# Kernel tuning notes

Hardware: AMD Instinct MI355X
Metric: run time of the kernel (lower is better)

The kernel has to match this reference:

```python
import jax, jax.numpy as jnp
import numpy as np

T, B, H, I = 128, 128, 256, 256


def setup_inputs() -> dict:
    key = jax.random.key(0)
    ks = jax.random.split(key, 8)
    s = 1.0 / np.sqrt(H)
    embs = jax.random.normal(ks[0], (T, B, I), jnp.float32)
    # lens in [1, T] (a length of 0 is meaningless for this module)
    lens = jnp.maximum(jax.random.randint(ks[1], (B,), 0, T + 1), 1)
    Wih = jax.random.uniform(ks[2], (4 * H, I), jnp.float32, -s, s)
    Whh = jax.random.uniform(ks[3], (4 * H, H), jnp.float32, -s, s)
    bih = jax.random.uniform(ks[4], (4 * H,), jnp.float32, -s, s)
    bhh = jax.random.uniform(ks[5], (4 * H,), jnp.float32, -s, s)
    Wa = jax.random.uniform(ks[6], (H, 2 * H), jnp.float32, -s, s)
    ba = jnp.zeros((H,), jnp.float32)
    return {"embs": embs, "lens": lens, "Wih": Wih, "Whh": Whh,
            "bih": bih, "bhh": bhh, "Wa": Wa, "ba": ba}


def _forward(embs, Wih, Whh, bih, bhh, Wa, ba):
    Tn, Bn, _ = embs.shape
    Hn = Whh.shape[1]
    h0 = jnp.zeros((Bn, Hn), embs.dtype)
    c0 = jnp.zeros((Bn, Hn), embs.dtype)
    hids0 = jnp.zeros((Tn, Bn, Hn), embs.dtype)  # growing history of outputs
    pos = jnp.arange(Tn)

    def step(carry, emb):
        h, c, hids, t = carry
        # attention of current hidden over all previous outputs (dot-product scores)
        scores = jnp.einsum('bh,tbh->tb', h, hids)          # [T,B]
        valid = pos[:, None] < jnp.maximum(t, 1)             # at least one valid slot avoids NaN
        scores = jnp.where(valid, scores, -1e30)
        w = jax.nn.softmax(scores, axis=0)
        ctx = jnp.einsum('tb,tbh->bh', w, hids)              # [B,H]
        h_att = jnp.tanh(jnp.concatenate([h, ctx], axis=-1) @ Wa.T + ba)
        h_in = jnp.where(t > 0, h_att, h)                    # no attention before first output
        # one LSTM cell step (PyTorch gate order: i, f, g, o)
        gates = emb @ Wih.T + bih + h_in @ Whh.T + bhh       # [B,4H]
        i, f, g, o = jnp.split(gates, 4, axis=-1)
        c_new = jax.nn.sigmoid(f) * c + jax.nn.sigmoid(i) * jnp.tanh(g)
        h_new = jax.nn.sigmoid(o) * jnp.tanh(c_new)
        hids = jax.lax.dynamic_update_slice(hids, h_new[None], (t, 0, 0))
        return (h_new, c_new, hids, t + 1), (h_new, c_new)

    _, (hs, cs) = jax.lax.scan(step, (h0, c0, hids0, jnp.int32(0)), embs)
    return hs, cs  # each [T,B,H]


def reference(embs, lens, Wih, Whh, bih, bhh, Wa, ba):
    hs, cs = _forward(embs, Wih, Whh, bih, bhh, Wa, ba)
    bidx = jnp.arange(hs.shape[1])
    h_fin = hs[lens - 1, bidx][None]  # [1,B,H], state at t == len-1
    c_fin = cs[lens - 1, bidx][None]
    return hs, h_fin, c_fin
```

## Files before the change

kernel.cpp:

```cpp
#include <hip/hip_runtime.h>
#include <math.h>

#define T 128
#define B 128
#define H 256
#define I 256
#define G4 1024
#define NB 2

typedef unsigned short u16;
typedef unsigned int u32;

__device__ __forceinline__ float2 bf2_to_f2(u32 u) {
    union { u32 i; float f; } a, b;
    a.i = u << 16;
    b.i = u & 0xffff0000u;
    return make_float2(a.f, b.f);
}
__device__ __forceinline__ float bf1_to_f(u16 u) {
    union { u32 i; float f; } a; a.i = ((u32)u) << 16; return a.f;
}
__device__ __forceinline__ u16 bf16_rne(float f) {
    union { float f; u32 u; } x; x.f = f;
    u32 r = x.u + 0x7fffu + ((x.u >> 16) & 1u);
    return (u16)(r >> 16);
}
__device__ __forceinline__ float sigmoid_fast(float x) {
    return 1.0f / (1.0f + __expf(-x));
}
__device__ __forceinline__ float tanh_fast(float x) {
    x = fminf(fmaxf(x, -15.f), 15.f);
    const float e = __expf(2.0f * x);
    return (e - 1.0f) / (e + 1.0f);
}

__global__ void pack_whB(const float* __restrict__ Whh, u16* __restrict__ WhB) {
    const int k = blockIdx.x;
    const int o = threadIdx.x;
    WhB[(size_t)k * G4 + o] = bf16_rne(Whh[(size_t)o * H + k]);
}
__global__ void pack_waB(const float* __restrict__ Wa, u16* __restrict__ WaB) {
    const int k = blockIdx.x;
    const int j = threadIdx.x;
    WaB[(size_t)k * H + j] = bf16_rne(Wa[(size_t)j * (2 * H) + k]);
}

__global__ __launch_bounds__(256) void gemm_g(const float* __restrict__ A,
                                              const float* __restrict__ W,
                                              const float* __restrict__ bih,
                                              const float* __restrict__ bhh,
                                              float* __restrict__ G) {
    __shared__ __align__(16) float As[64][68];
    __shared__ __align__(16) float Ws[64][68];
    const int m0 = blockIdx.x * 64;
    const int n0 = blockIdx.y * 64;
    const int tid = threadIdx.x;
    const int ty = tid >> 4, tx = tid & 15;
    const int rr = tid >> 4;
    const int kr = tid & 15;

    float acc[4][4] = {};
    for (int k0 = 0; k0 < I; k0 += 64) {
#pragma unroll
        for (int i = 0; i < 4; ++i) {
            const int r = rr + 16 * i;
            const float4 av = *(const float4*)&A[(size_t)(m0 + r) * I + k0 + kr * 4];
            const float4 wv = *(const float4*)&W[(size_t)(n0 + r) * I + k0 + kr * 4];
            As[kr * 4 + 0][r] = av.x; As[kr * 4 + 1][r] = av.y;
            As[kr * 4 + 2][r] = av.z; As[kr * 4 + 3][r] = av.w;
            Ws[kr * 4 + 0][r] = wv.x; Ws[kr * 4 + 1][r] = wv.y;
            Ws[kr * 4 + 2][r] = wv.z; Ws[kr * 4 + 3][r] = wv.w;
        }
        __syncthreads();
#pragma unroll 8
        for (int kk = 0; kk < 64; ++kk) {
            const float4 a4 = *(const float4*)&As[kk][ty * 4];
            const float4 w4 = *(const float4*)&Ws[kk][tx * 4];
            const float a[4] = {a4.x, a4.y, a4.z, a4.w};
            const float w[4] = {w4.x, w4.y, w4.z, w4.w};
#pragma unroll
            for (int i = 0; i < 4; ++i)
#pragma unroll
                for (int jj = 0; jj < 4; ++jj)
                    acc[i][jj] = fmaf(a[i], w[jj], acc[i][jj]);
        }
        __syncthreads();
    }
    const int n = n0 + tx * 4;
    const float4 bi = *(const float4*)&bih[n];
    const float4 bh = *(const float4*)&bhh[n];
    const float4 bb = make_float4(bi.x + bh.x, bi.y + bh.y, bi.z + bh.z, bi.w + bh.w);
#pragma unroll
    for (int i = 0; i < 4; ++i) {
        const int m = m0 + ty * 4 + i;
        float4 o = make_float4(acc[i][0] + bb.x, acc[i][1] + bb.y,
                               acc[i][2] + bb.z, acc[i][3] + bb.w);
        *(float4*)&G[(size_t)m * G4 + n] = o;
    }
}

__global__ __launch_bounds__(1024, 4) void alstm3(
    const int* __restrict__ lens,
    const float* __restrict__ G,
    const u16* __restrict__ WhB,
    const u16* __restrict__ WaB,
    const float* __restrict__ ba,
    float* __restrict__ out)
{
    __shared__ __align__(16) u16   hid_s[NB][T][H];
    __shared__ __align__(16) float red_s[4096];
    __shared__ __align__(16) float gate_s[NB][G4];
    __shared__ __align__(16) float h_s[NB][H];
    __shared__ __align__(16) float hin_s[NB][H];
    __shared__ __align__(16) float ctx_s[NB][H];
    __shared__ __align__(16) float sc_s[NB][T];

    const int b0 = blockIdx.x * NB;
    const int tid = threadIdx.x;
    const int lane = tid & 63;
    const int wave = tid >> 6;
    const int sb = wave >> 3;
    const int stp0 = wave & 7;
    const int cb = tid >> 9;
    const int ck = (tid >> 8) & 1;
    const int cj = tid & 255;
    const int ako = tid >> 7;
    const int aj = (tid & 127) * 2;
    const int hko = tid >> 9;
    const int ho = (tid & 511) * 2;
    const int eb = tid >> 8;
    const int ej = tid & 255;

    const int len0 = lens[b0], len1 = lens[b0 + 1];
    float c_reg = 0.f;
    if (tid < NB * H) h_s[eb][ej] = 0.f;
    float* hfin = out + (size_t)T * B * H;
    float* cfin = hfin + (size_t)B * H;
    __syncthreads();

    for (int t = 0; t < T; ++t) {
        const float gA = G[((size_t)t * B + b0) * G4 + tid];
        const float gB = G[((size_t)t * B + b0 + 1) * G4 + tid];

        if (t > 0) {
            const float4 h4 = *(const float4*)&h_s[sb][lane * 4];
            for (int tp = stp0; tp < t; tp += 8) {
                const uint2 hv = *(const uint2*)&hid_s[sb][tp][lane * 4];
                const float2 ha = bf2_to_f2(hv.x);
                const float2 hb = bf2_to_f2(hv.y);
                float d = ha.x * h4.x + ha.y * h4.y + hb.x * h4.z + hb.y * h4.w;
#pragma unroll
                for (int off = 32; off; off >>= 1) d += __shfl_xor(d, off);
                if (lane == 0) sc_s[sb][tp] = d;
            }
            __syncthreads();
            if (stp0 == 0) {
                const float v0 = (lane < t) ? sc_s[sb][lane] : -3.0e38f;
                const float v1 = (lane + 64 < t) ? sc_s[sb][lane + 64] : -3.0e38f;
                float m = fmaxf(v0, v1);
#pragma unroll
                for (int off = 32; off; off >>= 1) m = fmaxf(m, __shfl_xor(m, off));
                const float e0 = (lane < t) ? __expf(v0 - m) : 0.f;
                const float e1 = (lane + 64 < t) ? __expf(v1 - m) : 0.f;
                float s = e0 + e1;
#pragma unroll
                for (int off = 32; off; off >>= 1) s += __shfl_xor(s, off);
                const float inv = 1.f / s;
                if (lane < t) sc_s[sb][lane] = e0 * inv;
                if (lane + 64 < t) sc_s[sb][lane + 64] = e1 * inv;
            }
            __syncthreads();
            {
                float cacc = 0.f;
#pragma unroll 4
                for (int tp = ck; tp < t; tp += 2)
                    cacc = fmaf(sc_s[cb][tp], bf1_to_f(hid_s[cb][tp][cj]), cacc);
                red_s[cb * 512 + ck * 256 + cj] = cacc;
                gate_s[0][tid] = gA;
                gate_s[1][tid] = gB;
            }
            __syncthreads();
            if (tid < 512)
                ctx_s[eb][ej] = red_s[eb * 512 + ej] + red_s[eb * 512 + 256 + ej];
            __syncthreads();
            {
                const float* base0 = (ako < 4) ? &h_s[0][ako * 64] : &ctx_s[0][ako * 64 - 256];
                const float* base1 = (ako < 4) ? &h_s[1][ako * 64] : &ctx_s[1][ako * 64 - 256];
                const u16* wp = &WaB[(size_t)(ako * 64) * H + aj];
                float a00 = 0.f, a01 = 0.f, a10 = 0.f, a11 = 0.f;
#pragma unroll 8
                for (int kk = 0; kk < 64; ++kk) {
                    const u32 w = *(const u32*)(wp + (size_t)kk * H);
                    const float2 wv = bf2_to_f2(w);
                    const float v0 = base0[kk];
                    const float v1 = base1[kk];
                    a00 = fmaf(wv.x, v0, a00); a01 = fmaf(wv.y, v0, a01);
                    a10 = fmaf(wv.x, v1, a10); a11 = fmaf(wv.y, v1, a11);
                }
                *(float2*)&red_s[ako * 512 + aj] = make_float2(a00, a01);
                *(float2*)&red_s[ako * 512 + 256 + aj] = make_float2(a10, a11);
            }
            __syncthreads();
            if (tid < 512) {
                float a = ba[ej];
#pragma unroll
                for (int r = 0; r < 8; ++r) a += red_s[r * 512 + eb * 256 + ej];
                hin_s[eb][ej] = tanh_fast(a);
            }
            __syncthreads();
        } else {
            gate_s[0][tid] = gA;
            gate_s[1][tid] = gB;
            if (tid < 512) hin_s[eb][ej] = 0.f;
            __syncthreads();
        }
        {
            const u16* wp = &WhB[(size_t)(hko * 128) * G4 + ho];
            float a00 = 0.f, a01 = 0.f, a10 = 0.f, a11 = 0.f;
#pragma unroll 8
            for (int kk = 0; kk < 128; ++kk) {
                const int k = hko * 128 + kk;
                const u32 w = *(const u32*)(wp + (size_t)kk * G4);
                const float2 wv = bf2_to_f2(w);
                const float h0 = hin_s[0][k];
                const float h1 = hin_s[1][k];
                a00 = fmaf(wv.x, h0, a00); a01 = fmaf(wv.y, h0, a01);
                a10 = fmaf(wv.x, h1, a10); a11 = fmaf(wv.y, h1, a11);
            }
            *(float2*)&red_s[hko * 2048 + ho] = make_float2(a00, a01);
            *(float2*)&red_s[hko * 2048 + 1024 + ho] = make_float2(a10, a11);
        }
        __syncthreads();
        if (tid < 512) {
            const int bg = b0 + eb;
            const float gi = gate_s[eb][ej] + red_s[eb * 1024 + ej] + red_s[2048 + eb * 1024 + ej];
            const float gf = gate_s[eb][H + ej] + red_s[eb * 1024 + H + ej] + red_s[2048 + eb * 1024 + H + ej];
            const float gg = gate_s[eb][2 * H + ej] + red_s[eb * 1024 + 2 * H + ej] + red_s[2048 + eb * 1024 + 2 * H + ej];
            const float go = gate_s[eb][3 * H + ej] + red_s[eb * 1024 + 3 * H + ej] + red_s[2048 + eb * 1024 + 3 * H + ej];
            const float ig = sigmoid_fast(gi);
            const float fg = sigmoid_fast(gf);
            const float gv = tanh_fast(gg);
            const float og = sigmoid_fast(go);
            c_reg = fmaf(fg, c_reg, ig * gv);
            const float h_new = og * tanh_fast(c_reg);
            h_s[eb][ej] = h_new;
            hid_s[eb][t][ej] = bf16_rne(h_new);
            out[((size_t)t * B + bg) * H + ej] = h_new;
            const int lb = eb ? len1 : len0;
            if (t == lb - 1) {
                hfin[(size_t)bg * H + ej] = h_new;
                cfin[(size_t)bg * H + ej] = c_reg;
            }
        }
        __syncthreads();
    }
}

extern "C" void kernel_launch(void* const* d_in, const int* in_sizes, int n_in,
                              void* d_out, int out_size, void* d_ws, size_t ws_size,
                              hipStream_t stream) {
    const float* embs = (const float*)d_in[0];
    const int*   lens = (const int*)d_in[1];
    const float* Wih  = (const float*)d_in[2];
    const float* Whh  = (const float*)d_in[3];
    const float* bih  = (const float*)d_in[4];
    const float* bhh  = (const float*)d_in[5];
    const float* Wa   = (const float*)d_in[6];
    const float* ba   = (const float*)d_in[7];
    float* out = (float*)d_out;

    float* G  = (float*)d_ws;
    u16* WhB  = (u16*)(G + (size_t)T * B * G4);
    u16* WaB  = WhB + (size_t)H * G4;

    pack_whB<<<H, G4, 0, stream>>>(Whh, WhB);
    pack_waB<<<2 * H, H, 0, stream>>>(Wa, WaB);
    dim3 ggrid(T * B / 64, G4 / 64);
    gemm_g<<<ggrid, 256, 0, stream>>>(embs, Wih, bih, bhh, G);
    alstm3<<<B / NB, 1024, 0, stream>>>(lens, G, WhB, WaB, ba, out);
}
```

Baseline: 2.043 ms.

## Switch recurrent weights and history to fp16 with packed dot2 instructions

Replaces the bf16 storage of recurrent weights, attention weights and hidden history with fp16 pairs packed along the reduction dimension. The matvecs now use the v_dot2 fp32-accumulate instruction, with activations interleaved for the two batch rows so that one weight load serves both. Each thread covers a full output column, which removes the split-K partial sums and shrinks the reduction buffer. This cuts ALU work and bf16 unpacking per step, in exchange for fp16 range and precision limits on weights and hidden states.

```diff
diff --git a/kernel.cpp b/kernel.cpp
--- a/kernel.cpp
+++ b/kernel.cpp
@@ -10,21 +10,24 @@
 
 typedef unsigned short u16;
 typedef unsigned int u32;
-
-__device__ __forceinline__ float2 bf2_to_f2(u32 u) {
-    union { u32 i; float f; } a, b;
-    a.i = u << 16;
-    b.i = u & 0xffff0000u;
-    return make_float2(a.f, b.f);
-}
-__device__ __forceinline__ float bf1_to_f(u16 u) {
-    union { u32 i; float f; } a; a.i = ((u32)u) << 16; return a.f;
-}
-__device__ __forceinline__ u16 bf16_rne(float f) {
-    union { float f; u32 u; } x; x.f = f;
-    u32 r = x.u + 0x7fffu + ((x.u >> 16) & 1u);
-    return (u16)(r >> 16);
-}
+typedef _Float16 half_t;
+typedef _Float16 half2_t __attribute__((ext_vector_type(2)));
+
+#if defined(__has_builtin)
+#if __has_builtin(__builtin_amdgcn_fdot2)
+#define HAS_FDOT2 1
+#endif
+#endif
+
+__device__ __forceinline__ float fdot2(half2_t a, half2_t b, float c) {
+#ifdef HAS_FDOT2
+    return __builtin_amdgcn_fdot2(a, b, c, false);
+#else
+    return fmaf((float)a.x, (float)b.x, fmaf((float)a.y, (float)b.y, c));
+#endif
+}
+__device__ __forceinline__ half2_t h2cast(u32 u) { return __builtin_bit_cast(half2_t, u); }
+
 __device__ __forceinline__ float sigmoid_fast(float x) {
     return 1.0f / (1.0f + __expf(-x));
 }
@@ -34,15 +37,21 @@
     return (e - 1.0f) / (e + 1.0f);
 }
 
-__global__ void pack_whB(const float* __restrict__ Whh, u16* __restrict__ WhB) {
-    const int k = blockIdx.x;
-    const int o = threadIdx.x;
-    WhB[(size_t)k * G4 + o] = bf16_rne(Whh[(size_t)o * H + k]);
-}
-__global__ void pack_waB(const float* __restrict__ Wa, u16* __restrict__ WaB) {
-    const int k = blockIdx.x;
-    const int j = threadIdx.x;
-    WaB[(size_t)k * H + j] = bf16_rne(Wa[(size_t)j * (2 * H) + k]);
+__global__ void pack_whH(const float* __restrict__ Whh, half2_t* __restrict__ WhH) {
+    const int k2 = blockIdx.x;
+    const int o  = threadIdx.x;
+    half2_t v;
+    v.x = (half_t)Whh[(size_t)o * H + 2 * k2];
+    v.y = (half_t)Whh[(size_t)o * H + 2 * k2 + 1];
+    WhH[(size_t)k2 * G4 + o] = v;
+}
+__global__ void pack_waH(const float* __restrict__ Wa, half2_t* __restrict__ WaH) {
+    const int k2 = blockIdx.x;
+    const int j  = threadIdx.x;
+    half2_t v;
+    v.x = (half_t)Wa[(size_t)j * (2 * H) + 2 * k2];
+    v.y = (half_t)Wa[(size_t)j * (2 * H) + 2 * k2 + 1];
+    WaH[(size_t)k2 * H + j] = v;
 }
 
 __global__ __launch_bounds__(256) void gemm_g(const float* __restrict__ A,
@@ -99,21 +108,21 @@
     }
 }
 
-__global__ __launch_bounds__(1024, 4) void alstm3(
+__global__ __launch_bounds__(1024, 4) void alstm4(
     const int* __restrict__ lens,
     const float* __restrict__ G,
-    const u16* __restrict__ WhB,
-    const u16* __restrict__ WaB,
+    const half2_t* __restrict__ WhH,
+    const half2_t* __restrict__ WaH,
     const float* __restrict__ ba,
     float* __restrict__ out)
 {
-    __shared__ __align__(16) u16   hid_s[NB][T][H];
-    __shared__ __align__(16) float red_s[4096];
-    __shared__ __align__(16) float gate_s[NB][G4];
-    __shared__ __align__(16) float h_s[NB][H];
-    __shared__ __align__(16) float hin_s[NB][H];
-    __shared__ __align__(16) float ctx_s[NB][H];
-    __shared__ __align__(16) float sc_s[NB][T];
+    __shared__ __align__(16) half_t hid_s[NB][T][H];
+    __shared__ __align__(16) float  sc_s[NB][T];
+    __shared__ __align__(16) half_t hH_s[NB][H];
+    __shared__ __align__(16) half_t hcI_s[4 * 256];
+    __shared__ __align__(16) half_t hinI_s[4 * 128];
+    __shared__ __align__(16) float  red_s[2048];
+    __shared__ __align__(16) float  gate_s[NB][G4];
 
     const int b0 = blockIdx.x * NB;
     const int tid = threadIdx.x;
@@ -124,18 +133,16 @@
     const int cb = tid >> 9;
     const int ck = (tid >> 8) & 1;
     const int cj = tid & 255;
-    const int ako = tid >> 7;
-    const int aj = (tid & 127) * 2;
-    const int hko = tid >> 9;
-    const int ho = (tid & 511) * 2;
+    const int ako = tid >> 8;
+    const int aj = tid & 255;
     const int eb = tid >> 8;
     const int ej = tid & 255;
 
     const int len0 = lens[b0], len1 = lens[b0 + 1];
     float c_reg = 0.f;
-    if (tid < NB * H) h_s[eb][ej] = 0.f;
     float* hfin = out + (size_t)T * B * H;
     float* cfin = hfin + (size_t)B * H;
+    if (tid < 512) hH_s[eb][ej] = (half_t)0.f;
     __syncthreads();
 
     for (int t = 0; t < T; ++t) {
@@ -143,12 +150,11 @@
         const float gB = G[((size_t)t * B + b0 + 1) * G4 + tid];
 
         if (t > 0) {
-            const float4 h4 = *(const float4*)&h_s[sb][lane * 4];
+            const half2_t h2a = h2cast(*(const u32*)&hH_s[sb][lane * 4]);
+            const half2_t h2b = h2cast(*(const u32*)&hH_s[sb][lane * 4 + 2]);
             for (int tp = stp0; tp < t; tp += 8) {
                 const uint2 hv = *(const uint2*)&hid_s[sb][tp][lane * 4];
-                const float2 ha = bf2_to_f2(hv.x);
-                const float2 hb = bf2_to_f2(hv.y);
-                float d = ha.x * h4.x + ha.y * h4.y + hb.x * h4.z + hb.y * h4.w;
+                float d = fdot2(h2cast(hv.x), h2a, fdot2(h2cast(hv.y), h2b, 0.f));
 #pragma unroll
                 for (int off = 32; off; off >>= 1) d += __shfl_xor(d, off);
                 if (lane == 0) sc_s[sb][tp] = d;
@@ -172,79 +178,76 @@
             __syncthreads();
             {
                 float cacc = 0.f;
-#pragma unroll 4
                 for (int tp = ck; tp < t; tp += 2)
-                    cacc = fmaf(sc_s[cb][tp], bf1_to_f(hid_s[cb][tp][cj]), cacc);
+                    cacc = fmaf(sc_s[cb][tp], (float)hid_s[cb][tp][cj], cacc);
                 red_s[cb * 512 + ck * 256 + cj] = cacc;
                 gate_s[0][tid] = gA;
                 gate_s[1][tid] = gB;
             }
             __syncthreads();
-            if (tid < 512)
-                ctx_s[eb][ej] = red_s[eb * 512 + ej] + red_s[eb * 512 + 256 + ej];
+            if (tid < 512) {
+                const float ctxv = red_s[eb * 512 + ej] + red_s[eb * 512 + 256 + ej];
+                hcI_s[512 + 4 * (ej >> 1) + 2 * eb + (ej & 1)] = (half_t)ctxv;
+            }
             __syncthreads();
             {
-                const float* base0 = (ako < 4) ? &h_s[0][ako * 64] : &ctx_s[0][ako * 64 - 256];
-                const float* base1 = (ako < 4) ? &h_s[1][ako * 64] : &ctx_s[1][ako * 64 - 256];
-                const u16* wp = &WaB[(size_t)(ako * 64) * H + aj];
-                float a00 = 0.f, a01 = 0.f, a10 = 0.f, a11 = 0.f;
+                const half2_t* wp = &WaH[(size_t)(ako * 64) * H + aj];
+                float a0 = 0.f, a1 = 0.f;
 #pragma unroll 8
                 for (int kk = 0; kk < 64; ++kk) {
-                    const u32 w = *(const u32*)(wp + (size_t)kk * H);
-                    const float2 wv = bf2_to_f2(w);
-                    const float v0 = base0[kk];
-                    const float v1 = base1[kk];
-                    a00 = fmaf(wv.x, v0, a00); a01 = fmaf(wv.y, v0, a01);
-                    a10 = fmaf(wv.x, v1, a10); a11 = fmaf(wv.y, v1, a11);
+                    const int k2 = ako * 64 + kk;
+                    const uint2 hh = *(const uint2*)&hcI_s[4 * k2];
+                    const half2_t w = wp[(size_t)kk * H];
+                    a0 = fdot2(w, h2cast(hh.x), a0);
+                    a1 = fdot2(w, h2cast(hh.y), a1);
                 }
-                *(float2*)&red_s[ako * 512 + aj] = make_float2(a00, a01);
-                *(float2*)&red_s[ako * 512 + 256 + aj] = make_float2(a10, a11);
+                red_s[ako * 512 + aj] = a0;
+                red_s[ako * 512 + 256 + aj] = a1;
             }
             __syncthreads();
             if (tid < 512) {
                 float a = ba[ej];
 #pragma unroll
-                for (int r = 0; r < 8; ++r) a += red_s[r * 512 + eb * 256 + ej];
-                hin_s[eb][ej] = tanh_fast(a);
+                for (int r = 0; r < 4; ++r) a += red_s[r * 512 + eb * 256 + ej];
+                hinI_s[4 * (ej >> 1) + 2 * eb + (ej & 1)] = (half_t)tanh_fast(a);
             }
             __syncthreads();
         } else {
             gate_s[0][tid] = gA;
             gate_s[1][tid] = gB;
-            if (tid < 512) hin_s[eb][ej] = 0.f;
+            if (tid < 512) hinI_s[tid] = (half_t)0.f;
             __syncthreads();
         }
         {
-            const u16* wp = &WhB[(size_t)(hko * 128) * G4 + ho];
-            float a00 = 0.f, a01 = 0.f, a10 = 0.f, a11 = 0.f;
+            const half2_t* wp = &WhH[tid];
+            float g0 = 0.f, g1 = 0.f;
 #pragma unroll 8
-            for (int kk = 0; kk < 128; ++kk) {
-                const int k = hko * 128 + kk;
-                const u32 w = *(const u32*)(wp + (size_t)kk * G4);
-                const float2 wv = bf2_to_f2(w);
-                const float h0 = hin_s[0][k];
-                const float h1 = hin_s[1][k];
-                a00 = fmaf(wv.x, h0, a00); a01 = fmaf(wv.y, h0, a01);
-                a10 = fmaf(wv.x, h1, a10); a11 = fmaf(wv.y, h1, a11);
-            }
-            *(float2*)&red_s[hko * 2048 + ho] = make_float2(a00, a01);
-            *(float2*)&red_s[hko * 2048 + 1024 + ho] = make_float2(a10, a11);
+            for (int k2 = 0; k2 < 128; ++k2) {
+                const uint2 hh = *(const uint2*)&hinI_s[4 * k2];
+                const half2_t w = wp[(size_t)k2 * G4];
+                g0 = fdot2(w, h2cast(hh.x), g0);
+                g1 = fdot2(w, h2cast(hh.y), g1);
+            }
+            red_s[tid] = g0;
+            red_s[1024 + tid] = g1;
         }
         __syncthreads();
         if (tid < 512) {
             const int bg = b0 + eb;
-            const float gi = gate_s[eb][ej] + red_s[eb * 1024 + ej] + red_s[2048 + eb * 1024 + ej];
-            const float gf = gate_s[eb][H + ej] + red_s[eb * 1024 + H + ej] + red_s[2048 + eb * 1024 + H + ej];
-            const float gg = gate_s[eb][2 * H + ej] + red_s[eb * 1024 + 2 * H + ej] + red_s[2048 + eb * 1024 + 2 * H + ej];
-            const float go = gate_s[eb][3 * H + ej] + red_s[eb * 1024 + 3 * H + ej] + red_s[2048 + eb * 1024 + 3 * H + ej];
+            const float gi = gate_s[eb][ej]           + red_s[eb * 1024 + ej];
+            const float gf = gate_s[eb][H + ej]       + red_s[eb * 1024 + H + ej];
+            const float gg = gate_s[eb][2 * H + ej]   + red_s[eb * 1024 + 2 * H + ej];
+            const float go = gate_s[eb][3 * H + ej]   + red_s[eb * 1024 + 3 * H + ej];
             const float ig = sigmoid_fast(gi);
             const float fg = sigmoid_fast(gf);
             const float gv = tanh_fast(gg);
             const float og = sigmoid_fast(go);
             c_reg = fmaf(fg, c_reg, ig * gv);
             const float h_new = og * tanh_fast(c_reg);
-            h_s[eb][ej] = h_new;
-            hid_s[eb][t][ej] = bf16_rne(h_new);
+            const half_t hh = (half_t)h_new;
+            hH_s[eb][ej] = hh;
+            hid_s[eb][t][ej] = hh;
+            hcI_s[4 * (ej >> 1) + 2 * eb + (ej & 1)] = hh;
             out[((size_t)t * B + bg) * H + ej] = h_new;
             const int lb = eb ? len1 : len0;
             if (t == lb - 1) {
@@ -269,13 +272,13 @@
     const float* ba   = (const float*)d_in[7];
     float* out = (float*)d_out;
 
-    float* G  = (float*)d_ws;
-    u16* WhB  = (u16*)(G + (size_t)T * B * G4);
-    u16* WaB  = WhB + (size_t)H * G4;
-
-    pack_whB<<<H, G4, 0, stream>>>(Whh, WhB);
-    pack_waB<<<2 * H, H, 0, stream>>>(Wa, WaB);
+    float* G      = (float*)d_ws;
+    half2_t* WhH  = (half2_t*)(G + (size_t)T * B * G4);
+    half2_t* WaH  = WhH + (size_t)128 * G4;
+
+    pack_whH<<<128, G4, 0, stream>>>(Whh, WhH);
+    pack_waH<<<256, H, 0, stream>>>(Wa, WaH);
     dim3 ggrid(T * B / 64, G4 / 64);
     gemm_g<<<ggrid, 256, 0, stream>>>(embs, Wih, bih, bhh, G);
-    alstm3<<<B / NB, 1024, 0, stream>>>(lens, G, WhB, WaB, ba, out);
-}
+    alstm4<<<B / NB, 1024, 0, stream>>>(lens, G, WhH, WaH, ba, out);
+}
```

Result: faster. 1.886 ms (-7.7%).
